# Optimization experiments

Measured on AMD Instinct MI355X. Metric: run time of the kernel, lower is better.

Reference implementation:

```python
import jax, jax.numpy as jnp
import numpy as np

EPS_DIV = 1e-6    # safe_div clamp
EPS_NORM = 1e-12  # F.normalize eps
EPS_PD = 1e-6     # F.pairwise_distance eps (added to the difference)


def setup_inputs() -> dict:
    key = jax.random.key(0)
    k1, k2, k3 = jax.random.split(key, 3)
    B, N, D, C = 8, 2048, 512, 8192
    x = jax.random.normal(k1, (B, N, D), dtype=jnp.float32)
    W = jax.random.normal(k2, (D, D), dtype=jnp.float32) * (1.0 / np.sqrt(D))
    codebook = jax.random.normal(k3, (C, D), dtype=jnp.float32)
    return {"x": x, "W": W, "codebook": codebook}


def reference(x, W, codebook):
    sg = jax.lax.stop_gradient
    # implicit codebook = Linear(dim, dim, bias=False)(codebook)  -> codebook @ W^T
    imp = codebook @ W.T                                  # [C, D]

    lead = x.shape[:-1]
    D = x.shape[-1]
    xf = x.reshape(-1, D)                                 # [T, D]

    # nearest-neighbor search (no_grad in original): squared-dist argmin == cdist argmin
    d2 = (jnp.sum(xf * xf, axis=-1, keepdims=True)
          - 2.0 * (xf @ imp.T)
          + jnp.sum(imp * imp, axis=-1)[None, :])         # [T, C]
    indices = jnp.argmin(sg(d2), axis=-1)                 # [T]

    qf = imp[indices]                                     # [T, D] gather

    # commit loss: (pairwise_distance(x, q.detach())**2).mean(); torch adds eps to the diff
    diff = xf - sg(qf) + EPS_PD
    commit_loss = jnp.mean(jnp.sum(diff * diff, axis=-1))

    # rotation trick
    norm_x = jnp.linalg.norm(xf, axis=-1, keepdims=True)  # [T, 1]
    norm_q = jnp.linalg.norm(qf, axis=-1, keepdims=True)
    u = xf / jnp.maximum(norm_x, EPS_DIV)
    q = qf / jnp.maximum(norm_q, EPS_DIV)
    s = u + q
    w = sg(s / jnp.maximum(jnp.linalg.norm(s, axis=-1, keepdims=True), EPS_NORM))
    e = xf
    # e - 2 (e.w) w + 2 (e.u_sg) q_sg   (rank-1 products per row)
    rot = (e
           - 2.0 * jnp.sum(e * w, axis=-1, keepdims=True) * w
           + 2.0 * jnp.sum(e * sg(u), axis=-1, keepdims=True) * sg(q))
    quantized = rot * sg(norm_q / jnp.maximum(norm_x, EPS_DIV))

    quantized = quantized.reshape(*lead, D)
    indices = indices.reshape(*lead)
    return quantized, indices, commit_loss
```

## Files before the change

### kernel.cpp

```cpp
#include <hip/hip_runtime.h>
#include <cstdint>
#include <cstddef>

#define DD 512
#define TT 16384
#define CC 8192
#define SPLITC 32
#define EPS_DIV 1e-6f
#define EPS_NORM 1e-12f
#define EPS_PD 1e-6f

typedef _Float16 half8 __attribute__((ext_vector_type(8)));
typedef _Float16 half4 __attribute__((ext_vector_type(4)));
typedef float floatx4 __attribute__((ext_vector_type(4)));

#define GLDS16(g, l) __builtin_amdgcn_global_load_lds( \
    (const __attribute__((address_space(1))) void*)(g), \
    (__attribute__((address_space(3))) void*)(l), 16, 0, 0)

__global__ __launch_bounds__(128) void k_split(const float* __restrict__ src,
                                               _Float16* __restrict__ dst) {
  const int row = blockIdx.x;
  const int col = threadIdx.x * 4;
  float4 v = *(const float4*)(src + (size_t)row * DD + col);
  half4 h, l;
  h.x = (_Float16)v.x; l.x = (_Float16)(v.x - (float)h.x);
  h.y = (_Float16)v.y; l.y = (_Float16)(v.y - (float)h.y);
  h.z = (_Float16)v.z; l.z = (_Float16)(v.z - (float)h.z);
  h.w = (_Float16)v.w; l.w = (_Float16)(v.w - (float)h.w);
  *(half4*)(dst + (size_t)row * 1024 + col) = h;
  *(half4*)(dst + (size_t)row * 1024 + 512 + col) = l;
}

__global__ __launch_bounds__(128) void k_cast16(const float* __restrict__ src,
                                                _Float16* __restrict__ dst) {
  const int row = blockIdx.x;
  const int col = threadIdx.x * 4;
  float4 v = *(const float4*)(src + (size_t)row * DD + col);
  half4 h;
  h.x = (_Float16)v.x; h.y = (_Float16)v.y;
  h.z = (_Float16)v.z; h.w = (_Float16)v.w;
  *(half4*)(dst + (size_t)row * DD + col) = h;
}

__global__ __launch_bounds__(256) void k_gemm_mfma(
    const _Float16* __restrict__ cbs, const _Float16* __restrict__ Ws,
    float* __restrict__ imp, _Float16* __restrict__ ih) {
  __shared__ __align__(16) char smem[65536];
  const int tid = threadIdx.x;
  const int w = tid >> 6, lane = tid & 63;
  const int quad = lane >> 4, l15 = lane & 15;
  const int wm = (w & 1) * 64, wn = (w >> 1) * 64;
  const int c0 = blockIdx.x * 128;
  const int n0 = blockIdx.y * 128;

  const int srow8 = lane >> 3;
  const int scol = ((lane & 7) ^ srow8) << 3;
  size_t arow[4], brow[4];
#pragma unroll
  for (int j = 0; j < 4; ++j) {
    arow[j] = (size_t)(c0 + j * 32 + w * 8 + srow8) * 1024 + scol;
    brow[j] = (size_t)(n0 + j * 32 + w * 8 + srow8) * 1024 + scol;
  }
  int aoff[4], boff[4];
#pragma unroll
  for (int i = 0; i < 4; ++i) {
    aoff[i] = ((wm + i * 16 + l15) * 64 + ((quad ^ (l15 & 7)) << 3)) * 2;
    boff[i] = ((wn + i * 16 + l15) * 64 + ((quad ^ (l15 & 7)) << 3)) * 2;
  }

  auto stage = [&](int buf, int ak, int bk) {
    char* ab = smem + buf * 32768;
    char* bb = ab + 16384;
#pragma unroll
    for (int j = 0; j < 4; ++j) {
      GLDS16(cbs + arow[j] + ak, (_Float16*)ab + (j * 32 + w * 8) * 64);
      GLDS16(Ws  + brow[j] + bk, (_Float16*)bb + (j * 32 + w * 8) * 64);
    }
  };

  floatx4 acc[4][4] = {};
  stage(0, 0, 0);
#pragma unroll 2
  for (int it = 0; it < 24; ++it) {
    __syncthreads();
    if (it < 23) {
      const int n = it + 1;
      const int p = n >> 3, kk = n & 7;
      const int ak = ((p == 2) ? 512 : 0) + kk * 64;
      const int bk = ((p == 1) ? 512 : 0) + kk * 64;
      stage(n & 1, ak, bk);
    }
    const char* ab = smem + (it & 1) * 32768;
    const char* bb = ab + 16384;
#pragma unroll
    for (int ks = 0; ks < 2; ++ks) {
      const int kx = ks * 64;
      half8 a[4], b[4];
#pragma unroll
      for (int mi = 0; mi < 4; ++mi)
        a[mi] = *(const half8*)(ab + (aoff[mi] ^ kx));
#pragma unroll
      for (int ni = 0; ni < 4; ++ni)
        b[ni] = *(const half8*)(bb + (boff[ni] ^ kx));
#pragma unroll
      for (int mi = 0; mi < 4; ++mi)
#pragma unroll
        for (int ni = 0; ni < 4; ++ni)
          acc[mi][ni] = __builtin_amdgcn_mfma_f32_16x16x32_f16(
              a[mi], b[ni], acc[mi][ni], 0, 0, 0);
    }
  }
#pragma unroll
  for (int mi = 0; mi < 4; ++mi)
#pragma unroll
    for (int r = 0; r < 4; ++r) {
      const int c = c0 + wm + mi * 16 + quad * 4 + r;
#pragma unroll
      for (int ni = 0; ni < 4; ++ni) {
        const int d = n0 + wn + ni * 16 + l15;
        const float v = acc[mi][ni][r];
        imp[(size_t)c * DD + d] = v;
        ih[(size_t)c * DD + d] = (_Float16)v;
      }
    }
}

__global__ __launch_bounds__(256) void k_row_norm2(
    const float* __restrict__ imp, float* __restrict__ cnorm) {
  const int lane = threadIdx.x & 63;
  const int row = blockIdx.x * 4 + (threadIdx.x >> 6);
  const float* p = imp + (size_t)row * DD + lane * 8;
  float4 a = *(const float4*)p;
  float4 b = *(const float4*)(p + 4);
  float s = a.x * a.x + a.y * a.y + a.z * a.z + a.w * a.w +
            b.x * b.x + b.y * b.y + b.z * b.z + b.w * b.w;
#pragma unroll
  for (int m = 1; m < 64; m <<= 1) s += __shfl_xor(s, m);
  if (lane == 0) cnorm[row] = s;
}

__global__ __launch_bounds__(512, 2) void k_dist_top2(
    const _Float16* __restrict__ xh, const _Float16* __restrict__ ih,
    const float* __restrict__ cnorm,
    float* __restrict__ bval, int* __restrict__ bidx) {
  __shared__ __align__(16) char smem[131072];
  const int tid = threadIdx.x;
  const int w = tid >> 6, lane = tid & 63;
  const int quad = lane >> 4, l15 = lane & 15;
  const int wr = w >> 2, wc = w & 3;
  const int r0 = blockIdx.x * 256;
  const int c0 = blockIdx.y * 256;

  const int rloc = lane >> 2;
  const int chunk = (lane & 3) ^ (rloc & 3) ^ ((rloc >> 2) & 3);
  const _Float16* pA0 = xh + (size_t)(r0 + w * 32 + rloc) * DD + chunk * 8;
  const _Float16* pA1 = pA0 + (size_t)16 * DD;
  const _Float16* pB0 = ih + (size_t)(c0 + w * 32 + rloc) * DD + chunk * 8;
  const _Float16* pB1 = pB0 + (size_t)16 * DD;
  const int ldsA0 = (w * 32) * 64;
  const int ldsA1 = ldsA0 + 16 * 64;
  const int ldsB0 = 16384 + ldsA0;
  const int ldsB1 = 16384 + ldsA1;

  const int slot = (quad ^ (l15 & 3) ^ ((l15 >> 2) & 3)) << 4;
  int aoff[8], boff[4];
#pragma unroll
  for (int mi = 0; mi < 8; ++mi)
    aoff[mi] = (wr * 128 + mi * 16 + l15) * 64 + slot;
#pragma unroll
  for (int ni = 0; ni < 4; ++ni)
    boff[ni] = 16384 + (wc * 64 + ni * 16 + l15) * 64 + slot;

  float cn[4];
#pragma unroll
  for (int ni = 0; ni < 4; ++ni)
    cn[ni] = cnorm[c0 + wc * 64 + ni * 16 + l15];

  floatx4 acc[8][4] = {};
  half8 a[8], bX[4], bY[4];

  auto STAGE = [&](int t) {
    char* base = smem + (t & 3) * 32768;
    const size_t ko = (size_t)(t * 32);
    GLDS16(pA0 + ko, base + ldsA0);
    GLDS16(pA1 + ko, base + ldsA1);
    GLDS16(pB0 + ko, base + ldsB0);
    GLDS16(pB1 + ko, base + ldsB1);
  };

  STAGE(0); STAGE(1); STAGE(2);
  asm volatile("s_waitcnt vmcnt(8)" ::: "memory");
  __builtin_amdgcn_s_barrier();
  __builtin_amdgcn_sched_barrier(0);
  {
    const char* ab = smem;
#pragma unroll
    for (int mi = 0; mi < 8; ++mi) a[mi] = *(const half8*)(ab + aoff[mi]);
#pragma unroll
    for (int ni = 0; ni < 4; ++ni) bX[ni] = *(const half8*)(ab + boff[ni]);
  }

#define K_ITER(T, BCUR, BNXT, DO_STAGE, VMC, DO_READ)                          \
  {                                                                            \
    if (DO_STAGE) STAGE((T) + 3);                                              \
    asm volatile("s_waitcnt vmcnt(" #VMC ")" ::: "memory");                    \
    __builtin_amdgcn_s_barrier();                                              \
    __builtin_amdgcn_sched_barrier(0);                                         \
    asm volatile("s_waitcnt lgkmcnt(0)" ::: "memory");                         \
    __builtin_amdgcn_sched_barrier(0);                                         \
    const char* nb = smem + (((T) + 1) & 3) * 32768;                           \
    __builtin_amdgcn_s_setprio(1);                                             \
    _Pragma("unroll")                                                          \
    for (int mi = 0; mi < 8; ++mi) {                                           \
      _Pragma("unroll")                                                        \
      for (int ni = 0; ni < 4; ++ni)                                           \
        acc[mi][ni] = __builtin_amdgcn_mfma_f32_16x16x32_f16(                  \
            a[mi], BCUR[ni], acc[mi][ni], 0, 0, 0);                            \
      if (DO_READ) a[mi] = *(const half8*)(nb + aoff[mi]);                     \
    }                                                                          \
    if (DO_READ) {                                                             \
      _Pragma("unroll")                                                        \
      for (int ni = 0; ni < 4; ++ni)                                           \
        BNXT[ni] = *(const half8*)(nb + boff[ni]);                             \
    }                                                                          \
    __builtin_amdgcn_s_setprio(0);                                             \
  }

  K_ITER(0,  bX, bY, true,  8, true)
  K_ITER(1,  bY, bX, true,  8, true)
  K_ITER(2,  bX, bY, true,  8, true)
  K_ITER(3,  bY, bX, true,  8, true)
  K_ITER(4,  bX, bY, true,  8, true)
  K_ITER(5,  bY, bX, true,  8, true)
  K_ITER(6,  bX, bY, true,  8, true)
  K_ITER(7,  bY, bX, true,  8, true)
  K_ITER(8,  bX, bY, true,  8, true)
  K_ITER(9,  bY, bX, true,  8, true)
  K_ITER(10, bX, bY, true,  8, true)
  K_ITER(11, bY, bX, true,  8, true)
  K_ITER(12, bX, bY, true,  8, true)
  K_ITER(13, bY, bX, false, 4, true)
  K_ITER(14, bX, bY, false, 0, true)
  K_ITER(15, bY, bX, false, 0, false)
#undef K_ITER

  __syncthreads();
  float* rv = (float*)smem;
  int* ri = (int*)(smem + 65536);
#pragma unroll
  for (int mi = 0; mi < 8; ++mi)
#pragma unroll
    for (int r = 0; r < 4; ++r) {
      const int row = wr * 128 + mi * 16 + quad * 4 + r;
      float bv = 3.4e38f; int bi = 0x7fffffff;
#pragma unroll
      for (int ni = 0; ni < 4; ++ni) {
        const float v = fmaf(-2.0f, acc[mi][ni][r], cn[ni]);
        const int c = c0 + wc * 64 + ni * 16 + l15;
        if (v < bv) { bv = v; bi = c; }
      }
      const int e = wc * 16 + l15;
      const int g = (row & 31) ^ ((row & 4) << 2);
      const int col = e ^ g;
      rv[row * 64 + col] = bv;
      ri[row * 64 + col] = bi;
    }
  __syncthreads();
  {
    const int row = tid >> 1, h = tid & 1;
    const int g = (row & 31) ^ ((row & 4) << 2);
    float v1 = 3.4e38f, v2 = 3.4e38f;
    int i1 = 0x7fffffff, i2 = 0x7fffffff;
#pragma unroll
    for (int j = 0; j < 32; ++j) {
      const int e = h * 32 + j;
      const int col = e ^ g;
      const float v = rv[row * 64 + col];
      const int i = ri[row * 64 + col];
      if (v < v1 || (v == v1 && i < i1)) { v2 = v1; i2 = i1; v1 = v; i1 = i; }
      else if (v < v2 || (v == v2 && i < i2)) { v2 = v; i2 = i; }
    }
    const float w1 = __shfl_xor(v1, 1), w2 = __shfl_xor(v2, 1);
    const int j1 = __shfl_xor(i1, 1), j2 = __shfl_xor(i2, 1);
    if (w1 < v1 || (w1 == v1 && j1 < i1)) {
      if (v1 < w2 || (v1 == w2 && i1 < j2)) { v2 = v1; i2 = i1; }
      else { v2 = w2; i2 = j2; }
      v1 = w1; i1 = j1;
    } else if (w1 < v2 || (w1 == v2 && j1 < i2)) { v2 = w1; i2 = j1; }
    if (h == 0) {
      const size_t o = ((size_t)blockIdx.y * TT + r0 + row) * 2;
      bval[o] = v1; bval[o + 1] = v2;
      bidx[o] = i1; bidx[o + 1] = i2;
    }
  }
}

__global__ __launch_bounds__(256) void k_epilogue(
    const float* __restrict__ x, const float* __restrict__ imp,
    const float* __restrict__ cnorm,
    const float* __restrict__ bval, const int* __restrict__ bidx,
    float* __restrict__ outq, float* __restrict__ outidx,
    float* __restrict__ rloss) {
  const int lane = threadIdx.x & 63;
  const int row = blockIdx.x * 4 + (threadIdx.x >> 6);
  float v1 = 3.4e38f, v2 = 3.4e38f;
  int i1 = 0x7fffffff, i2 = 0x7fffffff;
  if (lane < SPLITC) {
    const size_t o = ((size_t)lane * TT + row) * 2;
    v1 = bval[o]; v2 = bval[o + 1];
    i1 = bidx[o]; i2 = bidx[o + 1];
  }
#pragma unroll
  for (int m = 1; m < 64; m <<= 1) {
    const float w1 = __shfl_xor(v1, m), w2 = __shfl_xor(v2, m);
    const int j1 = __shfl_xor(i1, m), j2 = __shfl_xor(i2, m);
    if (w1 < v1 || (w1 == v1 && j1 < i1)) {
      if (v1 < w2 || (v1 == w2 && i1 < j2)) { v2 = v1; i2 = i1; }
      else { v2 = w2; i2 = j2; }
      v1 = w1; i1 = j1;
    } else {
      if (w1 < v2 || (w1 == v2 && j1 < i2)) { v2 = w1; i2 = j1; }
    }
  }
  const float* xr = x + (size_t)row * DD + lane * 8;
  float e[8], qa[8], qb[8];
  *(float4*)&e[0] = *(const float4*)xr;
  *(float4*)&e[4] = *(const float4*)(xr + 4);
  const float* q1p = imp + (size_t)i1 * DD + lane * 8;
  const float* q2p = imp + (size_t)i2 * DD + lane * 8;
  *(float4*)&qa[0] = *(const float4*)q1p;
  *(float4*)&qa[4] = *(const float4*)(q1p + 4);
  *(float4*)&qb[0] = *(const float4*)q2p;
  *(float4*)&qb[4] = *(const float4*)(q2p + 4);
  float d1 = 0.f, d2 = 0.f;
#pragma unroll
  for (int k = 0; k < 8; ++k) {
    d1 = fmaf(e[k], qa[k], d1);
    d2 = fmaf(e[k], qb[k], d2);
  }
#pragma unroll
  for (int m = 1; m < 64; m <<= 1) {
    d1 += __shfl_xor(d1, m);
    d2 += __shfl_xor(d2, m);
  }
  const float s1 = fmaf(-2.0f, d1, cnorm[i1]);
  const float s2 = fmaf(-2.0f, d2, cnorm[i2]);
  const bool use2 = (s2 < s1) || (s2 == s1 && i2 < i1);
  const int idx = use2 ? i2 : i1;
  float q[8];
#pragma unroll
  for (int k = 0; k < 8; ++k) q[k] = use2 ? qb[k] : qa[k];

  float xx = 0.f, qq = 0.f, xq = 0.f, cl = 0.f;
#pragma unroll
  for (int k = 0; k < 8; ++k) {
    xx = fmaf(e[k], e[k], xx);
    qq = fmaf(q[k], q[k], qq);
    xq = fmaf(e[k], q[k], xq);
    float d = e[k] - q[k] + EPS_PD;
    cl = fmaf(d, d, cl);
  }
#pragma unroll
  for (int m = 1; m < 64; m <<= 1) {
    xx += __shfl_xor(xx, m);
    qq += __shfl_xor(qq, m);
    xq += __shfl_xor(xq, m);
    cl += __shfl_xor(cl, m);
  }
  const float nx = sqrtf(xx), nq = sqrtf(qq);
  const float dx = fmaxf(nx, EPS_DIV), dq = fmaxf(nq, EPS_DIV);
  const float uu = xx / (dx * dx);
  const float qq2 = qq / (dq * dq);
  const float uq = xq / (dx * dq);
  const float ss = uu + qq2 + 2.0f * uq;
  const float dn = fmaxf(sqrtf(ss), EPS_NORM);
  const float es = xx / dx + xq / dq;
  const float a = 2.0f * es / (dn * dn);
  const float b = 2.0f * (xx / dx);
  const float scale = nq / dx;

  float ov[8];
#pragma unroll
  for (int k = 0; k < 8; ++k) {
    const float qp = q[k] / dq;
    const float sk = e[k] / dx + qp;
    ov[k] = (e[k] - a * sk + b * qp) * scale;
  }
  float* op = outq + (size_t)row * DD + lane * 8;
  *(float4*)op = *(const float4*)&ov[0];
  *(float4*)(op + 4) = *(const float4*)&ov[4];
  if (lane == 0) {
    outidx[row] = (float)idx;
    rloss[row] = cl;
  }
}

__global__ __launch_bounds__(256) void k_loss_final(
    const float* __restrict__ rloss, float* __restrict__ out) {
  __shared__ double red[256];
  const int tid = threadIdx.x;
  double s = 0.0;
  for (int i = tid; i < TT; i += 256) s += (double)rloss[i];
  red[tid] = s;
  __syncthreads();
  for (int st = 128; st > 0; st >>= 1) {
    if (tid < st) red[tid] += red[tid + st];
    __syncthreads();
  }
  if (tid == 0) out[0] = (float)(red[0] / (double)TT);
}

extern "C" void kernel_launch(void* const* d_in, const int* in_sizes, int n_in,
                              void* d_out, int out_size, void* d_ws, size_t ws_size,
                              hipStream_t stream) {
  const float* x  = (const float*)d_in[0];
  const float* W  = (const float*)d_in[1];
  const float* cb = (const float*)d_in[2];
  float* out = (float*)d_out;

  float* imp = (float*)d_ws;
  _Float16* ih = (_Float16*)(imp + (size_t)CC * DD);
  _Float16* cbs = ih + (size_t)CC * DD;
  _Float16* xh = cbs;
  _Float16* Ws = cbs + (size_t)CC * 1024;
  float* cnorm = (float*)(Ws + (size_t)DD * 1024);
  float* bval  = cnorm + CC;
  int*   bidx  = (int*)(bval + (size_t)SPLITC * TT * 2);
  float* rloss = (float*)(bidx + (size_t)SPLITC * TT * 2);

  float* out_q    = out;
  float* out_idx  = out + (size_t)TT * DD;
  float* out_loss = out_idx + TT;

  k_split<<<CC, 128, 0, stream>>>(cb, cbs);
  k_split<<<DD, 128, 0, stream>>>(W, Ws);
  k_gemm_mfma<<<dim3(CC / 128, DD / 128), 256, 0, stream>>>(cbs, Ws, imp, ih);
  k_row_norm2<<<CC / 4, 256, 0, stream>>>(imp, cnorm);
  k_cast16<<<TT, 128, 0, stream>>>(x, xh);
  k_dist_top2<<<dim3(TT / 256, CC / 256), 512, 0, stream>>>(xh, ih, cnorm, bval, bidx);
  k_epilogue<<<TT / 4, 256, 0, stream>>>(x, imp, cnorm, bval, bidx, out_q, out_idx, rloss);
  k_loss_final<<<1, 256, 0, stream>>>(rloss, out_loss);
}
```

Baseline: 343.9 us.

## Split distance GEMM K-loop into two half-tile phases with new LDS swizzle

Restructures the fp16 MFMA main loop of the distance/top-2 kernel into two phases per K-step, each computing half the M rows. It interleaves split A/B global-to-LDS staging with the phases and adds an extra barrier per step. The LDS layout moves from 64-byte rows to 128-byte rows holding two rows each, with an 8-way XOR swizzle, to cut bank conflicts and lower register pressure. The cost is twice as many barriers and lgkmcnt waits per K-step, which may expose LDS latency that the earlier prefetch-ahead reads hid.

```diff
diff --git a/kernel.cpp b/kernel.cpp
--- a/kernel.cpp
+++ b/kernel.cpp
@@ -152,25 +152,21 @@
   const int r0 = blockIdx.x * 256;
   const int c0 = blockIdx.y * 256;
 
-  const int rloc = lane >> 2;
-  const int chunk = (lane & 3) ^ (rloc & 3) ^ ((rloc >> 2) & 3);
-  const _Float16* pA0 = xh + (size_t)(r0 + w * 32 + rloc) * DD + chunk * 8;
-  const _Float16* pA1 = pA0 + (size_t)16 * DD;
-  const _Float16* pB0 = ih + (size_t)(c0 + w * 32 + rloc) * DD + chunk * 8;
-  const _Float16* pB1 = pB0 + (size_t)16 * DD;
-  const int ldsA0 = (w * 32) * 64;
-  const int ldsA1 = ldsA0 + 16 * 64;
-  const int ldsB0 = 16384 + ldsA0;
-  const int ldsB1 = 16384 + ldsA1;
-
-  const int slot = (quad ^ (l15 & 3) ^ ((l15 >> 2) & 3)) << 4;
+  const int se = (lane & 7) ^ ((lane >> 3) & 7);
+  const int rl = 2 * (lane >> 3) + ((se >> 2) & 1);
+  const int chh = (se & 3) * 8;
+  const _Float16* gA = xh + (size_t)(r0 + w * 32 + rl) * DD + chh;
+  const _Float16* gB = ih + (size_t)(c0 + w * 32 + rl) * DD + chh;
+  const int ldsW = w * 2048;
+
+  const int s8 = (((((l15 & 1) << 2) | quad) ^ ((l15 >> 1) & 7))) << 4;
   int aoff[8], boff[4];
 #pragma unroll
   for (int mi = 0; mi < 8; ++mi)
-    aoff[mi] = (wr * 128 + mi * 16 + l15) * 64 + slot;
+    aoff[mi] = (wr * 64 + mi * 8 + (l15 >> 1)) * 128 + s8;
 #pragma unroll
   for (int ni = 0; ni < 4; ++ni)
-    boff[ni] = 16384 + (wc * 64 + ni * 16 + l15) * 64 + slot;
+    boff[ni] = 16384 + (wc * 32 + ni * 8 + (l15 >> 1)) * 128 + s8;
 
   float cn[4];
 #pragma unroll
@@ -178,72 +174,88 @@
     cn[ni] = cnorm[c0 + wc * 64 + ni * 16 + l15];
 
   floatx4 acc[8][4] = {};
-  half8 a[8], bX[4], bY[4];
-
-  auto STAGE = [&](int t) {
-    char* base = smem + (t & 3) * 32768;
-    const size_t ko = (size_t)(t * 32);
-    GLDS16(pA0 + ko, base + ldsA0);
-    GLDS16(pA1 + ko, base + ldsA1);
-    GLDS16(pB0 + ko, base + ldsB0);
-    GLDS16(pB1 + ko, base + ldsB1);
+  half8 aA[4], aB[4], bf[4];
+
+  auto STAGE_A = [&](int t) {
+    char* d = smem + (t & 3) * 32768 + ldsW;
+    const _Float16* g = gA + (size_t)t * 32;
+    GLDS16(g, d);
+    GLDS16(g + (size_t)16 * DD, d + 1024);
   };
-
-  STAGE(0); STAGE(1); STAGE(2);
+  auto STAGE_B = [&](int t) {
+    char* d = smem + (t & 3) * 32768 + 16384 + ldsW;
+    const _Float16* g = gB + (size_t)t * 32;
+    GLDS16(g, d);
+    GLDS16(g + (size_t)16 * DD, d + 1024);
+  };
+
+  STAGE_A(0); STAGE_B(0);
+  STAGE_A(1); STAGE_B(1);
+  STAGE_A(2); STAGE_B(2);
   asm volatile("s_waitcnt vmcnt(8)" ::: "memory");
   __builtin_amdgcn_s_barrier();
   __builtin_amdgcn_sched_barrier(0);
-  {
-    const char* ab = smem;
-#pragma unroll
-    for (int mi = 0; mi < 8; ++mi) a[mi] = *(const half8*)(ab + aoff[mi]);
-#pragma unroll
-    for (int ni = 0; ni < 4; ++ni) bX[ni] = *(const half8*)(ab + boff[ni]);
-  }
-
-#define K_ITER(T, BCUR, BNXT, DO_STAGE, VMC, DO_READ)                          \
-  {                                                                            \
-    if (DO_STAGE) STAGE((T) + 3);                                              \
+
+#define PH0(T, DS) {                                                           \
+    const char* bb = smem + ((T) & 3) * 32768;                                 \
+    _Pragma("unroll")                                                          \
+    for (int i = 0; i < 4; ++i) aA[i] = *(const half8*)(bb + aoff[i]);         \
+    _Pragma("unroll")                                                          \
+    for (int i = 0; i < 4; ++i) bf[i] = *(const half8*)(bb + boff[i]);         \
+    if (DS) STAGE_A((T) + 3);                                                  \
+    __builtin_amdgcn_s_barrier();                                              \
+    asm volatile("s_waitcnt lgkmcnt(0)" ::: "memory");                         \
+    __builtin_amdgcn_sched_barrier(0);                                         \
+    __builtin_amdgcn_s_setprio(1);                                             \
+    _Pragma("unroll")                                                          \
+    for (int mi = 0; mi < 4; ++mi)                                             \
+      _Pragma("unroll")                                                        \
+      for (int ni = 0; ni < 4; ++ni)                                           \
+        acc[mi][ni] = __builtin_amdgcn_mfma_f32_16x16x32_f16(                  \
+            aA[mi], bf[ni], acc[mi][ni], 0, 0, 0);                             \
+    __builtin_amdgcn_s_setprio(0);                                             \
+    __builtin_amdgcn_sched_barrier(0);                                         \
+  }
+
+#define PH1(T, DS, VMC) {                                                      \
+    const char* bb = smem + ((T) & 3) * 32768;                                 \
+    _Pragma("unroll")                                                          \
+    for (int i = 0; i < 4; ++i) aB[i] = *(const half8*)(bb + aoff[4 + i]);     \
+    asm volatile("s_waitcnt lgkmcnt(0)" ::: "memory");                         \
+    __builtin_amdgcn_sched_barrier(0);                                         \
+    if (DS) STAGE_B((T) + 3);                                                  \
     asm volatile("s_waitcnt vmcnt(" #VMC ")" ::: "memory");                    \
     __builtin_amdgcn_s_barrier();                                              \
     __builtin_amdgcn_sched_barrier(0);                                         \
-    asm volatile("s_waitcnt lgkmcnt(0)" ::: "memory");                         \
-    __builtin_amdgcn_sched_barrier(0);                                         \
-    const char* nb = smem + (((T) + 1) & 3) * 32768;                           \
     __builtin_amdgcn_s_setprio(1);                                             \
     _Pragma("unroll")                                                          \
-    for (int mi = 0; mi < 8; ++mi) {                                           \
+    for (int mi = 0; mi < 4; ++mi)                                             \
       _Pragma("unroll")                                                        \
       for (int ni = 0; ni < 4; ++ni)                                           \
-        acc[mi][ni] = __builtin_amdgcn_mfma_f32_16x16x32_f16(                  \
-            a[mi], BCUR[ni], acc[mi][ni], 0, 0, 0);                            \
-      if (DO_READ) a[mi] = *(const half8*)(nb + aoff[mi]);                     \
-    }                                                                          \
-    if (DO_READ) {                                                             \
-      _Pragma("unroll")                                                        \
-      for (int ni = 0; ni < 4; ++ni)                                           \
-        BNXT[ni] = *(const half8*)(nb + boff[ni]);                             \
-    }                                                                          \
+        acc[4 + mi][ni] = __builtin_amdgcn_mfma_f32_16x16x32_f16(              \
+            aB[mi], bf[ni], acc[4 + mi][ni], 0, 0, 0);                         \
     __builtin_amdgcn_s_setprio(0);                                             \
-  }
-
-  K_ITER(0,  bX, bY, true,  8, true)
-  K_ITER(1,  bY, bX, true,  8, true)
-  K_ITER(2,  bX, bY, true,  8, true)
-  K_ITER(3,  bY, bX, true,  8, true)
-  K_ITER(4,  bX, bY, true,  8, true)
-  K_ITER(5,  bY, bX, true,  8, true)
-  K_ITER(6,  bX, bY, true,  8, true)
-  K_ITER(7,  bY, bX, true,  8, true)
-  K_ITER(8,  bX, bY, true,  8, true)
-  K_ITER(9,  bY, bX, true,  8, true)
-  K_ITER(10, bX, bY, true,  8, true)
-  K_ITER(11, bY, bX, true,  8, true)
-  K_ITER(12, bX, bY, true,  8, true)
-  K_ITER(13, bY, bX, false, 4, true)
-  K_ITER(14, bX, bY, false, 0, true)
-  K_ITER(15, bY, bX, false, 0, false)
-#undef K_ITER
+    __builtin_amdgcn_sched_barrier(0);                                         \
+  }
+
+  PH0(0, 1)  PH1(0, 1, 8)
+  PH0(1, 1)  PH1(1, 1, 8)
+  PH0(2, 1)  PH1(2, 1, 8)
+  PH0(3, 1)  PH1(3, 1, 8)
+  PH0(4, 1)  PH1(4, 1, 8)
+  PH0(5, 1)  PH1(5, 1, 8)
+  PH0(6, 1)  PH1(6, 1, 8)
+  PH0(7, 1)  PH1(7, 1, 8)
+  PH0(8, 1)  PH1(8, 1, 8)
+  PH0(9, 1)  PH1(9, 1, 8)
+  PH0(10, 1) PH1(10, 1, 8)
+  PH0(11, 1) PH1(11, 1, 8)
+  PH0(12, 1) PH1(12, 1, 8)
+  PH0(13, 0) PH1(13, 0, 4)
+  PH0(14, 0) PH1(14, 0, 0)
+  PH0(15, 0) PH1(15, 0, 0)
+#undef PH0
+#undef PH1
 
   __syncthreads();
   float* rv = (float*)smem;
```

Result: no change. 338.5 us (-1.6%).

## Pre-swizzle operands into MFMA fragment layout and load directly to registers

Applied to the files above, without the earlier changes.

Adds a cast kernel that writes x and the implicit codebook in fp16, already laid out in per-lane MFMA fragment order. The distance GEMM then loads its fragments straight from global memory into registers with double buffering, replacing the LDS staging pipeline. The aim is to remove LDS traffic, bank-conflict swizzling and waitcnt/barrier overhead. In exchange the GEMM depends on L2 bandwidth and global-load latency hiding with only one tile of prefetch, and the codebook needs an extra cast pass.

```diff
diff --git a/kernel.cpp b/kernel.cpp
--- a/kernel.cpp
+++ b/kernel.cpp
@@ -32,20 +32,30 @@
   *(half4*)(dst + (size_t)row * 1024 + 512 + col) = l;
 }
 
-__global__ __launch_bounds__(128) void k_cast16(const float* __restrict__ src,
-                                                _Float16* __restrict__ dst) {
-  const int row = blockIdx.x;
-  const int col = threadIdx.x * 4;
-  float4 v = *(const float4*)(src + (size_t)row * DD + col);
-  half4 h;
-  h.x = (_Float16)v.x; h.y = (_Float16)v.y;
-  h.z = (_Float16)v.z; h.w = (_Float16)v.w;
-  *(half4*)(dst + (size_t)row * DD + col) = h;
+__global__ __launch_bounds__(256) void k_cast_frag(const float* __restrict__ src,
+                                                   _Float16* __restrict__ dst) {
+  const int rb = blockIdx.x, t = blockIdx.y;
+  const int lane = threadIdx.x & 63, s0 = threadIdx.x >> 6;
+  const int l15 = lane & 15, quad = lane >> 4;
+#pragma unroll
+  for (int s = 0; s < 4; ++s) {
+    const int slot = s0 * 4 + s;
+    const int row = rb * 256 + slot * 16 + l15;
+    const float* p = src + (size_t)row * DD + t * 32 + quad * 8;
+    float4 v0 = *(const float4*)p;
+    float4 v1 = *(const float4*)(p + 4);
+    half8 h;
+    h[0] = (_Float16)v0.x; h[1] = (_Float16)v0.y;
+    h[2] = (_Float16)v0.z; h[3] = (_Float16)v0.w;
+    h[4] = (_Float16)v1.x; h[5] = (_Float16)v1.y;
+    h[6] = (_Float16)v1.z; h[7] = (_Float16)v1.w;
+    *(half8*)(dst + (((size_t)rb * 16 + t) * 16 + slot) * 512 + lane * 8) = h;
+  }
 }
 
 __global__ __launch_bounds__(256) void k_gemm_mfma(
     const _Float16* __restrict__ cbs, const _Float16* __restrict__ Ws,
-    float* __restrict__ imp, _Float16* __restrict__ ih) {
+    float* __restrict__ imp) {
   __shared__ __align__(16) char smem[65536];
   const int tid = threadIdx.x;
   const int w = tid >> 6, lane = tid & 63;
@@ -119,9 +129,7 @@
 #pragma unroll
       for (int ni = 0; ni < 4; ++ni) {
         const int d = n0 + wn + ni * 16 + l15;
-        const float v = acc[mi][ni][r];
-        imp[(size_t)c * DD + d] = v;
-        ih[(size_t)c * DD + d] = (_Float16)v;
+        imp[(size_t)c * DD + d] = acc[mi][ni][r];
       }
     }
 }
@@ -141,7 +149,7 @@
 }
 
 __global__ __launch_bounds__(512, 2) void k_dist_top2(
-    const _Float16* __restrict__ xh, const _Float16* __restrict__ ih,
+    const _Float16* __restrict__ xA, const _Float16* __restrict__ ihB,
     const float* __restrict__ cnorm,
     float* __restrict__ bval, int* __restrict__ bidx) {
   __shared__ __align__(16) char smem[131072];
@@ -152,98 +160,57 @@
   const int r0 = blockIdx.x * 256;
   const int c0 = blockIdx.y * 256;
 
-  const int rloc = lane >> 2;
-  const int chunk = (lane & 3) ^ (rloc & 3) ^ ((rloc >> 2) & 3);
-  const _Float16* pA0 = xh + (size_t)(r0 + w * 32 + rloc) * DD + chunk * 8;
-  const _Float16* pA1 = pA0 + (size_t)16 * DD;
-  const _Float16* pB0 = ih + (size_t)(c0 + w * 32 + rloc) * DD + chunk * 8;
-  const _Float16* pB1 = pB0 + (size_t)16 * DD;
-  const int ldsA0 = (w * 32) * 64;
-  const int ldsA1 = ldsA0 + 16 * 64;
-  const int ldsB0 = 16384 + ldsA0;
-  const int ldsB1 = 16384 + ldsA1;
-
-  const int slot = (quad ^ (l15 & 3) ^ ((l15 >> 2) & 3)) << 4;
-  int aoff[8], boff[4];
-#pragma unroll
-  for (int mi = 0; mi < 8; ++mi)
-    aoff[mi] = (wr * 128 + mi * 16 + l15) * 64 + slot;
-#pragma unroll
-  for (int ni = 0; ni < 4; ++ni)
-    boff[ni] = 16384 + (wc * 64 + ni * 16 + l15) * 64 + slot;
-
-  float cn[4];
-#pragma unroll
-  for (int ni = 0; ni < 4; ++ni)
-    cn[ni] = cnorm[c0 + wc * 64 + ni * 16 + l15];
+  const _Float16* gA = xA + ((size_t)blockIdx.x * 256 + wr * 8) * 512 + lane * 8;
+  const _Float16* gB = ihB + ((size_t)blockIdx.y * 256 + wc * 4) * 512 + lane * 8;
 
   floatx4 acc[8][4] = {};
-  half8 a[8], bX[4], bY[4];
-
-  auto STAGE = [&](int t) {
-    char* base = smem + (t & 3) * 32768;
-    const size_t ko = (size_t)(t * 32);
-    GLDS16(pA0 + ko, base + ldsA0);
-    GLDS16(pA1 + ko, base + ldsA1);
-    GLDS16(pB0 + ko, base + ldsB0);
-    GLDS16(pB1 + ko, base + ldsB1);
-  };
-
-  STAGE(0); STAGE(1); STAGE(2);
-  asm volatile("s_waitcnt vmcnt(8)" ::: "memory");
-  __builtin_amdgcn_s_barrier();
-  __builtin_amdgcn_sched_barrier(0);
-  {
-    const char* ab = smem;
-#pragma unroll
-    for (int mi = 0; mi < 8; ++mi) a[mi] = *(const half8*)(ab + aoff[mi]);
-#pragma unroll
-    for (int ni = 0; ni < 4; ++ni) bX[ni] = *(const half8*)(ab + boff[ni]);
-  }
-
-#define K_ITER(T, BCUR, BNXT, DO_STAGE, VMC, DO_READ)                          \
-  {                                                                            \
-    if (DO_STAGE) STAGE((T) + 3);                                              \
-    asm volatile("s_waitcnt vmcnt(" #VMC ")" ::: "memory");                    \
+  half8 aP[8], bP[4], aQ[8], bQ[4];
+
+#define LOADF(AR, BR, T) {                                                     \
+    const _Float16* ga = gA + (size_t)(T) * 8192;                              \
+    const _Float16* gb = gB + (size_t)(T) * 8192;                              \
+    _Pragma("unroll")                                                          \
+    for (int i = 0; i < 8; ++i) AR[i] = *(const half8*)(ga + i * 512);         \
+    _Pragma("unroll")                                                          \
+    for (int i = 0; i < 4; ++i) BR[i] = *(const half8*)(gb + i * 512);         \
+  }
+#define MMF(AR, BR) {                                                          \
     __builtin_amdgcn_s_barrier();                                              \
-    __builtin_amdgcn_sched_barrier(0);                                         \
-    asm volatile("s_waitcnt lgkmcnt(0)" ::: "memory");                         \
-    __builtin_amdgcn_sched_barrier(0);                                         \
-    const char* nb = smem + (((T) + 1) & 3) * 32768;                           \
     __builtin_amdgcn_s_setprio(1);                                             \
     _Pragma("unroll")                                                          \
-    for (int mi = 0; mi < 8; ++mi) {                                           \
+    for (int mi = 0; mi < 8; ++mi)                                             \
       _Pragma("unroll")                                                        \
       for (int ni = 0; ni < 4; ++ni)                                           \
         acc[mi][ni] = __builtin_amdgcn_mfma_f32_16x16x32_f16(                  \
-            a[mi], BCUR[ni], acc[mi][ni], 0, 0, 0);                            \
-      if (DO_READ) a[mi] = *(const half8*)(nb + aoff[mi]);                     \
-    }                                                                          \
-    if (DO_READ) {                                                             \
-      _Pragma("unroll")                                                        \
-      for (int ni = 0; ni < 4; ++ni)                                           \
-        BNXT[ni] = *(const half8*)(nb + boff[ni]);                             \
-    }                                                                          \
+            AR[mi], BR[ni], acc[mi][ni], 0, 0, 0);                             \
     __builtin_amdgcn_s_setprio(0);                                             \
-  }
-
-  K_ITER(0,  bX, bY, true,  8, true)
-  K_ITER(1,  bY, bX, true,  8, true)
-  K_ITER(2,  bX, bY, true,  8, true)
-  K_ITER(3,  bY, bX, true,  8, true)
-  K_ITER(4,  bX, bY, true,  8, true)
-  K_ITER(5,  bY, bX, true,  8, true)
-  K_ITER(6,  bX, bY, true,  8, true)
-  K_ITER(7,  bY, bX, true,  8, true)
-  K_ITER(8,  bX, bY, true,  8, true)
-  K_ITER(9,  bY, bX, true,  8, true)
-  K_ITER(10, bX, bY, true,  8, true)
-  K_ITER(11, bY, bX, true,  8, true)
-  K_ITER(12, bX, bY, true,  8, true)
-  K_ITER(13, bY, bX, false, 4, true)
-  K_ITER(14, bX, bY, false, 0, true)
-  K_ITER(15, bY, bX, false, 0, false)
-#undef K_ITER
+    __builtin_amdgcn_sched_barrier(0);                                         \
+  }
+
+  LOADF(aP, bP, 0)
+  LOADF(aQ, bQ, 1)   MMF(aP, bP)
+  LOADF(aP, bP, 2)   MMF(aQ, bQ)
+  LOADF(aQ, bQ, 3)   MMF(aP, bP)
+  LOADF(aP, bP, 4)   MMF(aQ, bQ)
+  LOADF(aQ, bQ, 5)   MMF(aP, bP)
+  LOADF(aP, bP, 6)   MMF(aQ, bQ)
+  LOADF(aQ, bQ, 7)   MMF(aP, bP)
+  LOADF(aP, bP, 8)   MMF(aQ, bQ)
+  LOADF(aQ, bQ, 9)   MMF(aP, bP)
+  LOADF(aP, bP, 10)  MMF(aQ, bQ)
+  LOADF(aQ, bQ, 11)  MMF(aP, bP)
+  LOADF(aP, bP, 12)  MMF(aQ, bQ)
+  LOADF(aQ, bQ, 13)  MMF(aP, bP)
+  LOADF(aP, bP, 14)  MMF(aQ, bQ)
+  LOADF(aQ, bQ, 15)  MMF(aP, bP)
+  MMF(aQ, bQ)
+#undef LOADF
+#undef MMF
+
+  float cn[4];
+#pragma unroll
+  for (int ni = 0; ni < 4; ++ni)
+    cn[ni] = cnorm[c0 + wc * 64 + ni * 16 + l15];
 
   __syncthreads();
   float* rv = (float*)smem;
@@ -420,9 +387,9 @@
   float* out = (float*)d_out;
 
   float* imp = (float*)d_ws;
-  _Float16* ih = (_Float16*)(imp + (size_t)CC * DD);
-  _Float16* cbs = ih + (size_t)CC * DD;
-  _Float16* xh = cbs;
+  _Float16* ihB = (_Float16*)(imp + (size_t)CC * DD);
+  _Float16* cbs = ihB + (size_t)CC * DD;
+  _Float16* xA = cbs;
   _Float16* Ws = cbs + (size_t)CC * 1024;
   float* cnorm = (float*)(Ws + (size_t)DD * 1024);
   float* bval  = cnorm + CC;
@@ -435,10 +402,11 @@
 
   k_split<<<CC, 128, 0, stream>>>(cb, cbs);
   k_split<<<DD, 128, 0, stream>>>(W, Ws);
-  k_gemm_mfma<<<dim3(CC / 128, DD / 128), 256, 0, stream>>>(cbs, Ws, imp, ih);
+  k_gemm_mfma<<<dim3(CC / 128, DD / 128), 256, 0, stream>>>(cbs, Ws, imp);
   k_row_norm2<<<CC / 4, 256, 0, stream>>>(imp, cnorm);
-  k_cast16<<<TT, 128, 0, stream>>>(x, xh);
-  k_dist_top2<<<dim3(TT / 256, CC / 256), 512, 0, stream>>>(xh, ih, cnorm, bval, bidx);
+  k_cast_frag<<<dim3(CC / 256, 16), 256, 0, stream>>>(imp, ihB);
+  k_cast_frag<<<dim3(TT / 256, 16), 256, 0, stream>>>(x, xA);
+  k_dist_top2<<<dim3(TT / 256, CC / 256), 512, 0, stream>>>(xA, ihB, cnorm, bval, bidx);
   k_epilogue<<<TT / 4, 256, 0, stream>>>(x, imp, cnorm, bval, bidx, out_q, out_idx, rloss);
   k_loss_final<<<1, 256, 0, stream>>>(rloss, out_loss);
 }
```

Result: no change. 346.0 us (+0.6%).
